# Performance work log

Hardware: AMD Instinct MI355X
Metric: run time of the kernel (lower is better)

Reference implementation:

```python
import jax, jax.numpy as jnp
import numpy as np

FEATURE_SCALE = 0.25  # cfg.feature_scale
G = 4                 # deformable/offset groups
K = 3                 # deform kernel size
KK = K * K
PAD = 1


def conv2d(x, w, b=None):
    y = jax.lax.conv_general_dilated(x, w, (1, 1), ((PAD, PAD), (PAD, PAD)),
                                     dimension_numbers=('NCHW', 'OIHW', 'NCHW'))
    return y if b is None else y + b[None, :, None, None]


def bilinear_upsample_ac(x, fs):
    # F.interpolate(mode='bilinear', align_corners=True, scale_factor=fs)
    b, c, H, W = x.shape
    Ho, Wo = H * fs, W * fs
    sy = jnp.arange(Ho, dtype=x.dtype) * ((H - 1) / (Ho - 1))
    sx = jnp.arange(Wo, dtype=x.dtype) * ((W - 1) / (Wo - 1))
    y0 = jnp.clip(jnp.floor(sy).astype(jnp.int32), 0, H - 2)
    x0 = jnp.clip(jnp.floor(sx).astype(jnp.int32), 0, W - 2)
    wy = (sy - y0)[None, None, :, None]
    wx = (sx - x0)[None, None, None, :]
    rows = x[:, :, y0, :] * (1 - wy) + x[:, :, y0 + 1, :] * wy
    return rows[:, :, :, x0] * (1 - wx) + rows[:, :, :, x0 + 1] * wx


def deform_conv(x, offset, mask, w):
    # torchvision.ops.deform_conv2d, stride 1, pad 1, weight groups = 1,
    # offset/mask groups = G. offset layout: (b, G*KK*2, H, W), (dy, dx) pairs.
    b, C, H, W = x.shape
    Cg = C // G
    off = offset.reshape(b, G, KK, 2, H, W)
    ii = (jnp.arange(KK) // K).reshape(1, 1, KK, 1, 1).astype(x.dtype)
    jj = (jnp.arange(KK) % K).reshape(1, 1, KK, 1, 1).astype(x.dtype)
    ys = jnp.arange(H, dtype=x.dtype).reshape(1, 1, 1, H, 1)
    xs = jnp.arange(W, dtype=x.dtype).reshape(1, 1, 1, 1, W)
    py = ys - PAD + ii + off[:, :, :, 0]   # (b,G,KK,H,W)
    px = xs - PAD + jj + off[:, :, :, 1]
    xt = x.reshape(b, G, Cg, H, W).transpose(0, 1, 3, 4, 2)  # (b,G,H,W,Cg)
    y0f = jnp.floor(py)
    x0f = jnp.floor(px)
    wy = py - y0f
    wx = px - x0f
    y0 = y0f.astype(jnp.int32)
    x0 = x0f.astype(jnp.int32)
    bi = jnp.arange(b).reshape(b, 1, 1, 1, 1)
    gi = jnp.arange(G).reshape(1, G, 1, 1, 1)

    def corner(yi, xi, wgt):
        valid = ((yi >= 0) & (yi < H) & (xi >= 0) & (xi < W)).astype(x.dtype)
        v = xt[bi, gi, jnp.clip(yi, 0, H - 1), jnp.clip(xi, 0, W - 1)]  # (b,G,KK,H,W,Cg)
        return v * (wgt * valid)[..., None]

    s = (corner(y0, x0, (1 - wy) * (1 - wx)) + corner(y0, x0 + 1, (1 - wy) * wx)
         + corner(y0 + 1, x0, wy * (1 - wx)) + corner(y0 + 1, x0 + 1, wy * wx))
    s = s * mask.reshape(b, G, KK, H, W)[..., None]
    wr = w.reshape(w.shape[0], G, Cg, KK)
    return jnp.einsum('bgkhwc,ogck->bohw', s, wr)


def _align(sou_list, ref_list, params):
    cat_feat, offset_vs = [], []
    for i in (3, 2, 1):
        sou, ref = sou_list[i - 1], ref_list[i - 1]
        b, C, H, W = sou.shape
        Cg = C // G
        off_w, off_b, mod_w, mod_b, reg_w = params[i]
        off_in = jnp.concatenate([sou.reshape(b, G, Cg, H, W),
                                  ref.reshape(b, G, Cg, H, W)], axis=2)
        off_in = off_in.reshape(b * G, 2 * Cg, H, W)
        offset = conv2d(off_in, off_w, off_b).reshape(b, G * 2 * KK, H, W)
        rng = min(H, W) * 0.5 / 2
        offset_map = rng * 2 * jax.nn.sigmoid(offset) - rng
        modulator = 2.0 * jax.nn.sigmoid(conv2d(sou, mod_w, mod_b))
        feat = deform_conv(sou, offset_map, modulator, reg_w)
        fs = int(1 // (FEATURE_SCALE / 2 ** (i - 1)))
        oy = jnp.mean(offset_map[:, 0::2], axis=1, keepdims=True)
        ox = jnp.mean(offset_map[:, 1::2], axis=1, keepdims=True)
        ov = bilinear_upsample_ac(jnp.concatenate([oy, ox], axis=1), fs) * fs
        cat_feat.append(feat)
        offset_vs.append(ov)
    return tuple(cat_feat) + tuple(offset_vs)


def setup_inputs() -> dict:
    key = jax.random.key(0)
    ks = jax.random.split(key, 32)
    d = {}
    shapes = {1: (2, 64, 128, 128), 2: (2, 64, 64, 64), 3: (2, 64, 32, 32)}
    k = 0
    for i in (1, 2, 3):
        d[f'sou{i}'] = jax.random.normal(ks[k], shapes[i], jnp.float32); k += 1
        d[f'ref{i}'] = jax.random.normal(ks[k], shapes[i], jnp.float32); k += 1
    Cg = 64 // G
    for i in (1, 2, 3):
        d[f'off_w{i}'] = jax.random.normal(ks[k], (2 * KK, 2 * Cg, K, K), jnp.float32) * 0.05; k += 1
        d[f'off_b{i}'] = jax.random.normal(ks[k], (2 * KK,), jnp.float32) * 0.05; k += 1
        d[f'mod_w{i}'] = jax.random.normal(ks[k], (G * KK, 64, K, K), jnp.float32) * 0.05; k += 1
        d[f'mod_b{i}'] = jax.random.normal(ks[k], (G * KK,), jnp.float32) * 0.05; k += 1
        d[f'reg_w{i}'] = jax.random.normal(ks[k], (64, 64, K, K), jnp.float32) * 0.05; k += 1
    return d


def reference(sou1, sou2, sou3, ref1, ref2, ref3,
              off_w1, off_b1, mod_w1, mod_b1, reg_w1,
              off_w2, off_b2, mod_w2, mod_b2, reg_w2,
              off_w3, off_b3, mod_w3, mod_b3, reg_w3):
    params = {1: (off_w1, off_b1, mod_w1, mod_b1, reg_w1),
              2: (off_w2, off_b2, mod_w2, mod_b2, reg_w2),
              3: (off_w3, off_b3, mod_w3, mod_b3, reg_w3)}
    return _align([sou1, sou2, sou3], [ref1, ref2, ref3], params)
```

## Files before the change

### kernel.cpp

```cpp
#include <hip/hip_runtime.h>

typedef __attribute__((ext_vector_type(8))) short short8;
typedef __attribute__((ext_vector_type(4))) float f32x4;

__device__ __forceinline__ float sigmoidf_(float x) { return 1.f / (1.f + __expf(-x)); }
__device__ __forceinline__ unsigned bf16rne(float x) {
    unsigned b = __float_as_uint(x);
    return (b + 0x7FFFu + ((b >> 16) & 1u)) >> 16;
}


struct P {
    const float *sou0, *sou1, *sou2;
    const float *ref0, *ref1, *ref2;
    const float *ob0, *ob1, *ob2;
    const float *mb0, *mb1, *mb2;
    float* out;
    float* ws;
};

union U {
    uint4 u4; int4 i4; short8 s8; f32x4 f4;
};

__global__ __launch_bounds__(256) void repack_all(
    const float* __restrict__ ow0, const float* __restrict__ mw0, const float* __restrict__ rw0,
    const float* __restrict__ ow1, const float* __restrict__ mw1, const float* __restrict__ rw1,
    const float* __restrict__ ow2, const float* __restrict__ mw2, const float* __restrict__ rw2,
    float* __restrict__ dst) {
    const int lvl = blockIdx.y;
    const float* ow = lvl == 0 ? ow0 : (lvl == 1 ? ow1 : ow2);
    const float* mw = lvl == 0 ? mw0 : (lvl == 1 ? mw1 : mw2);
    const float* rw = lvl == 0 ? rw0 : (lvl == 1 ? rw1 : rw2);
    unsigned* d = (unsigned*)(dst + lvl * 62784);
    int i = blockIdx.x * 256 + threadIdx.x;
    if (i < 18432) {
        int jw = i & 3;
        int lane = (i >> 2) & 63;
        int t3 = i >> 8;
        int ks = t3 % 18, wvu = t3 / 18;
        int o = wvu * 16 + (lane & 15);
        int c0 = ks * 32 + (lane >> 4) * 8 + 2 * jw;
        int g0 = c0 / 144, r0 = c0 % 144;
        int c1 = c0 + 1;
        int g1 = c1 / 144, r1 = c1 % 144;
        float w0 = rw[o * 576 + (g0 * 16 + (r0 & 15)) * 9 + (r0 >> 4)];
        float w1 = rw[o * 576 + (g1 * 16 + (r1 & 15)) * 9 + (r1 >> 4)];
        d[i] = bf16rne(w0) | (bf16rne(w1) << 16);
    } else if (i < 23552) {
        int o2 = i - 18432;
        int jw = o2 & 3;
        int lane = (o2 >> 2) & 63;
        int t2 = o2 >> 8;
        int nt = t2 & 1;
        int hk = t2 >> 1;
        int ks = hk % 5, h = hk / 5;
        int n = nt * 16 + (lane & 15);
        int K = ks * 32 + (lane >> 4) * 8 + 2 * jw;
        int tap = K >> 4, ch = K & 15;
        bool ok = (n < 18) && (tap < 9);
        float w0 = ok ? ow[n * 288 + (h * 16 + ch) * 9 + tap] : 0.f;
        float w1 = ok ? ow[n * 288 + (h * 16 + ch + 1) * 9 + tap] : 0.f;
        d[36864 + o2] = bf16rne(w0) | (bf16rne(w1) << 16);
    } else if (i < 37376) {
        int o3 = i - 23552;
        int jw = o3 & 3;
        int lane = (o3 >> 2) & 63;
        int t3 = o3 >> 8;
        int nt = t3 % 3, tc = t3 / 3;
        int tap = tc >> 1, c = tc & 1;
        int n = nt * 16 + (lane & 15);
        int ic0 = c * 32 + (lane >> 4) * 8 + 2 * jw;
        float w0 = (n < 36) ? mw[n * 576 + ic0 * 9 + tap] : 0.f;
        float w1 = (n < 36) ? mw[n * 576 + (ic0 + 1) * 9 + tap] : 0.f;
        d[41984 + o3] = bf16rne(w0) | (bf16rne(w1) << 16);
    }
}

__global__ __launch_bounds__(256) void k1_prep(P p) {
    __shared__ __align__(16) char smem[28512];
    const int t = blockIdx.x;
    float* ws = p.ws;
    const int tid = threadIdx.x;

    int lvl, j;
    if (t < 512) { lvl = 0; j = t; }
    else if (t < 640) { lvl = 1; j = t - 512; }
    else { lvl = 2; j = t - 640; }
    const int logW = 7 - lvl;
    const int W = 1 << logW, H = W, HW = H * W;
    const int nper = 256 >> (2 * lvl);
    const int qb = j % nper, b = j / nper;
    const int q0 = qb * 64;
    const int hlo = q0 >> logW;
    const int xlo = q0 & (W - 1);
    const int cols = (W >= 64) ? 66 : 34;
    const int rcTot = (W >= 64) ? 198 : 136;
    const float* sou = lvl == 0 ? p.sou0 : (lvl == 1 ? p.sou1 : p.sou2);
    const float* ref = lvl == 0 ? p.ref0 : (lvl == 1 ? p.ref1 : p.ref2);
    const float* base_s = sou + (size_t)b * 64 * HW;
    const float* base_r = ref + (size_t)b * 64 * HW;
    unsigned* ldsW = (unsigned*)smem;
    const bool sact = tid < rcTot;
    const int srow = tid / cols, scol = tid - srow * cols;
    const int grow = hlo - 1 + srow, gcol = xlo - 1 + scol;
    const bool inb = sact && grow >= 0 && grow < H && gcol >= 0 && gcol < W;
    const size_t goff = inb ? ((size_t)grow * W + gcol) : 0;

    float v[32];
#pragma unroll
    for (int hb = 0; hb < 2; ++hb) {
#pragma unroll
        for (int c8 = 0; c8 < 4; ++c8) {
            const float* p0 = base_s + (size_t)((hb * 4 + c8) * 8) * HW;
#pragma unroll
            for (int jj = 0; jj < 8; ++jj)
                v[c8 * 8 + jj] = inb ? p0[(size_t)jj * HW + goff] : 0.f;
        }
        if (sact) {
#pragma unroll
            for (int c8 = 0; c8 < 4; ++c8) {
                uint4 wv;
                wv.x = bf16rne(v[c8 * 8 + 0]) | (bf16rne(v[c8 * 8 + 1]) << 16);
                wv.y = bf16rne(v[c8 * 8 + 2]) | (bf16rne(v[c8 * 8 + 3]) << 16);
                wv.z = bf16rne(v[c8 * 8 + 4]) | (bf16rne(v[c8 * 8 + 5]) << 16);
                wv.w = bf16rne(v[c8 * 8 + 6]) | (bf16rne(v[c8 * 8 + 7]) << 16);
                *(uint4*)&ldsW[tid * 36 + (hb * 4 + c8) * 4] = wv;
            }
        }
    }
    __syncthreads();

    unsigned* XTb = (unsigned*)(ws + 4919232) +
                    (lvl == 0 ? 0 : (lvl == 1 ? 1048576 : 1310720));
#pragma unroll
    for (int u = 0; u < 2; ++u) {
        const int idx = tid * 2 + u;
        const int px = idx >> 3, gh = idx & 7;
        const int g = gh >> 1, half = gh & 1;
        const int rc = ((px >> logW) + 1) * cols + (px & (W - 1)) + 1;
        uint4 vv = *(const uint4*)&ldsW[rc * 36 + g * 8 + half * 4];
        *(uint4*)(XTb + ((size_t)(b * 4 + g) * HW + q0 + px) * 8 + half * 4) = vv;
    }

    const int wvu = __builtin_amdgcn_readfirstlane(tid >> 6);
    const int lane = tid & 63, quad = lane >> 4, lo16 = lane & 15;
    const int qg = q0 + wvu * 16 + lo16;
    const int rowB = (qg >> logW) - hlo;
    const int colB = (qg & (W - 1)) - xlo;
    const unsigned short* ldsS = (const unsigned short*)smem;
    const unsigned* WREPu = (const unsigned*)(ws + 4730880 + lvl * 62784);
    const unsigned* WBO2 = WREPu + 36864;
    const unsigned* WBM = WREPu + 41984;

    f32x4 accM[3], accO[4][2];
#pragma unroll
    for (int nt = 0; nt < 3; ++nt) accM[nt] = (f32x4){0.f, 0.f, 0.f, 0.f};
#pragma unroll
    for (int g = 0; g < 4; ++g)
#pragma unroll
        for (int nt = 0; nt < 2; ++nt) accO[g][nt] = (f32x4){0.f, 0.f, 0.f, 0.f};

#pragma unroll
    for (int tap = 0; tap < 9; ++tap) {
        const int ky = tap / 3, kx = tap - ky * 3;
        const int rc = (rowB + ky) * cols + colB + kx;
#pragma unroll
        for (int c = 0; c < 2; ++c) {
            U au; au.s8 = *(const short8*)&ldsS[rc * 72 + c * 32 + quad * 8];
#pragma unroll
            for (int nt = 0; nt < 3; ++nt) {
                U bu;
                bu.u4 = *(const uint4*)(WBM + (((tap * 2 + c) * 3 + nt) * 64 + lane) * 4);
                accM[nt] = __builtin_amdgcn_mfma_f32_16x16x32_bf16(au.s8, bu.s8, accM[nt], 0, 0, 0);
            }
        }
    }
#pragma unroll
    for (int ks = 0; ks < 5; ++ks) {
        const int Kbase = ks * 32 + quad * 8;
        const int tap = min(Kbase >> 4, 8);
        const int ky = tap / 3, kx = tap - ky * 3;
        const int rc = (rowB + ky) * cols + colB + kx;
        const int choff = Kbase & 15;
        U bu0, bu1;
        bu0.u4 = *(const uint4*)(WBO2 + ((ks * 2 + 0) * 64 + lane) * 4);
        bu1.u4 = *(const uint4*)(WBO2 + ((ks * 2 + 1) * 64 + lane) * 4);
#pragma unroll
        for (int g = 0; g < 4; ++g) {
            U au; au.s8 = *(const short8*)&ldsS[rc * 72 + g * 16 + choff];
            accO[g][0] = __builtin_amdgcn_mfma_f32_16x16x32_bf16(au.s8, bu0.s8, accO[g][0], 0, 0, 0);
            accO[g][1] = __builtin_amdgcn_mfma_f32_16x16x32_bf16(au.s8, bu1.s8, accO[g][1], 0, 0, 0);
        }
    }
    __syncthreads();

#pragma unroll
    for (int hb = 0; hb < 2; ++hb) {
#pragma unroll
        for (int c8 = 0; c8 < 4; ++c8) {
            const float* p0 = base_r + (size_t)((hb * 4 + c8) * 8) * HW;
#pragma unroll
            for (int jj = 0; jj < 8; ++jj)
                v[c8 * 8 + jj] = inb ? p0[(size_t)jj * HW + goff] : 0.f;
        }
        if (sact) {
#pragma unroll
            for (int c8 = 0; c8 < 4; ++c8) {
                uint4 wv;
                wv.x = bf16rne(v[c8 * 8 + 0]) | (bf16rne(v[c8 * 8 + 1]) << 16);
                wv.y = bf16rne(v[c8 * 8 + 2]) | (bf16rne(v[c8 * 8 + 3]) << 16);
                wv.z = bf16rne(v[c8 * 8 + 4]) | (bf16rne(v[c8 * 8 + 5]) << 16);
                wv.w = bf16rne(v[c8 * 8 + 6]) | (bf16rne(v[c8 * 8 + 7]) << 16);
                *(uint4*)&ldsW[tid * 36 + (hb * 4 + c8) * 4] = wv;
            }
        }
        if (hb == 0) __syncthreads();
    }
    __syncthreads();

#pragma unroll
    for (int ks = 0; ks < 5; ++ks) {
        const int Kbase = ks * 32 + quad * 8;
        const int tap = min(Kbase >> 4, 8);
        const int ky = tap / 3, kx = tap - ky * 3;
        const int rc = (rowB + ky) * cols + colB + kx;
        const int choff = Kbase & 15;
        U bu0, bu1;
        bu0.u4 = *(const uint4*)(WBO2 + (((5 + ks) * 2 + 0) * 64 + lane) * 4);
        bu1.u4 = *(const uint4*)(WBO2 + (((5 + ks) * 2 + 1) * 64 + lane) * 4);
#pragma unroll
        for (int g = 0; g < 4; ++g) {
            U au; au.s8 = *(const short8*)&ldsS[rc * 72 + g * 16 + choff];
            accO[g][0] = __builtin_amdgcn_mfma_f32_16x16x32_bf16(au.s8, bu0.s8, accO[g][0], 0, 0, 0);
            accO[g][1] = __builtin_amdgcn_mfma_f32_16x16x32_bf16(au.s8, bu1.s8, accO[g][1], 0, 0, 0);
        }
    }

    {
        const float* bias = lvl == 0 ? p.mb0 : (lvl == 1 ? p.mb1 : p.mb2);
        float* MOD = ws + (lvl == 0 ? 3096576 : (lvl == 1 ? 4276224 : 4571136));
#pragma unroll
        for (int nt = 0; nt < 3; ++nt) {
            const int o = nt * 16 + lo16;
            if (o < 36) {
                const float bb = bias[o];
                float* op = MOD + (size_t)(b * 36 + o) * HW + q0 + wvu * 16 + quad * 4;
                *(float4*)op = make_float4(2.f * sigmoidf_(accM[nt][0] + bb),
                                           2.f * sigmoidf_(accM[nt][1] + bb),
                                           2.f * sigmoidf_(accM[nt][2] + bb),
                                           2.f * sigmoidf_(accM[nt][3] + bb));
            }
        }
    }
    {
        const float* bias = lvl == 0 ? p.ob0 : (lvl == 1 ? p.ob1 : p.ob2);
        float* OFFM = ws + (lvl == 0 ? 0 : (lvl == 1 ? 2359296 : 2949120));
        const float rng = 0.25f * (float)H;
        float macc[4] = {0.f, 0.f, 0.f, 0.f};
#pragma unroll
        for (int g = 0; g < 4; ++g)
#pragma unroll
            for (int nt = 0; nt < 2; ++nt) {
                const int o = nt * 16 + lo16;
                if (o < 18) {
                    const float bb = bias[o];
                    float ovv[4];
#pragma unroll
                    for (int rg = 0; rg < 4; ++rg)
                        ovv[rg] = rng * (2.f * sigmoidf_(accO[g][nt][rg] + bb) - 1.f);
                    float* op = OFFM + (size_t)(b * 72 + g * 18 + o) * HW + q0 + wvu * 16 + quad * 4;
                    *(float4*)op = make_float4(ovv[0], ovv[1], ovv[2], ovv[3]);
#pragma unroll
                    for (int rg = 0; rg < 4; ++rg) macc[rg] += ovv[rg];
                }
            }
        const bool odd = (lo16 & 1) != 0;
        float my[4], mx[4];
#pragma unroll
        for (int rg = 0; rg < 4; ++rg) {
            my[rg] = odd ? 0.f : macc[rg];
            mx[rg] = odd ? macc[rg] : 0.f;
        }
#pragma unroll
        for (int m = 1; m < 16; m <<= 1) {
#pragma unroll
            for (int rg = 0; rg < 4; ++rg) {
                my[rg] += __shfl_xor(my[rg], m);
                mx[rg] += __shfl_xor(mx[rg], m);
            }
        }
        if (lo16 == 0) {
            float* MEAN = ws + (lvl == 0 ? 4644864 : (lvl == 1 ? 4710400 : 4726784));
            const int pxb = q0 + wvu * 16 + quad * 4;
            const float inv = 1.f / 36.f;
            *(float4*)(MEAN + (size_t)(b * 2) * HW + pxb) =
                make_float4(my[0] * inv, my[1] * inv, my[2] * inv, my[3] * inv);
            *(float4*)(MEAN + (size_t)(b * 2 + 1) * HW + pxb) =
                make_float4(mx[0] * inv, mx[1] * inv, mx[2] * inv, mx[3] * inv);
        }
    }
}

__global__ __launch_bounds__(256) void k2_fused(P p) {
    __shared__ __align__(16) unsigned lds[32 * 100];
    const int t = blockIdx.x;
    float* ws = p.ws;
    const int tid = threadIdx.x;
    if (t < 1344) {
        const int x = t & 7, r = t >> 3;
        int lvl, u;
        if (r < 128) { lvl = 0; u = x + ((r >> 1) << 3); }
        else if (r < 160) { lvl = 1; u = x + (((r - 128) >> 1) << 3); }
        else { lvl = 2; u = x + (((r - 160) >> 1) << 3); }
        const int j = 2 * u + (r & 1);
        const int logW = 7 - lvl;
        const int W = 1 << logW, H = W, HW = H * W;
        const int nper = 512 >> (2 * lvl);
        const int qb = j % nper, b = j / nper;
        const int q0 = qb * 32;
        const float* OFFM = ws + (lvl == 0 ? 0 : (lvl == 1 ? 2359296 : 2949120));
        const float* MOD = ws + (lvl == 0 ? 3096576 : (lvl == 1 ? 4276224 : 4571136));
        const unsigned* XTb = (const unsigned*)(ws + 4919232) +
                              (lvl == 0 ? 0 : (lvl == 1 ? 1048576 : 1310720));
        const unsigned* WB = (const unsigned*)(ws + 4730880 + lvl * 62784);
        float* outp = p.out + (lvl == 0 ? 655360 : (lvl == 1 ? 131072 : 0));
        const int wvu = __builtin_amdgcn_readfirstlane(tid >> 6);
        const int lane = tid & 63, quad = lane >> 4, lo16 = lane & 15;
        f32x4 acc[2];
        acc[0] = (f32x4){0.f, 0.f, 0.f, 0.f};
        acc[1] = (f32x4){0.f, 0.f, 0.f, 0.f};
        for (int c = 0; c < 3; ++c) {
            if (c) __syncthreads();
#pragma unroll
            for (int it = 0; it < 2; ++it) {
                const int task = it * 256 + tid;
                if (task < 384) {
                    const int gkl = task >> 5, px = task & 31;
                    const int gk = c * 12 + gkl;
                    const int g = gk / 9, k = gk - g * 9;
                    const int q = q0 + px;
                    const int h = q >> logW, xp = q & (W - 1);
                    const int ky = k / 3, kx = k - ky * 3;
                    float dy = OFFM[(size_t)(b * 72 + g * 18 + 2 * k) * HW + q];
                    float dx = OFFM[(size_t)(b * 72 + g * 18 + 2 * k + 1) * HW + q];
                    float m = MOD[(size_t)(b * 36 + g * 9 + k) * HW + q];
                    float py = (float)(h - 1 + ky) + dy;
                    float pxx = (float)(xp - 1 + kx) + dx;
                    float y0f = floorf(py), x0f = floorf(pxx);
                    float wy = py - y0f, wx = pxx - x0f;
                    int y0 = (int)y0f, x0 = (int)x0f;
                    const unsigned* xg = XTb + (size_t)(b * 4 + g) * HW * 8;
                    float s[16];
#pragma unroll
                    for (int cc = 0; cc < 16; ++cc) s[cc] = 0.f;
#pragma unroll
                    for (int cor = 0; cor < 4; ++cor) {
                        int yy = y0 + (cor >> 1), xx = x0 + (cor & 1);
                        float cw = ((cor >> 1) ? wy : 1.f - wy) * ((cor & 1) ? wx : 1.f - wx);
                        cw = (yy >= 0 && yy < H && xx >= 0 && xx < W) ? cw * m : 0.f;
                        int yc = min(max(yy, 0), H - 1), xc = min(max(xx, 0), W - 1);
                        const uint4* cp = (const uint4*)(xg + (size_t)((yc << logW) + xc) * 8);
                        unsigned cbuf[8];
                        *(uint4*)&cbuf[0] = cp[0];
                        *(uint4*)&cbuf[4] = cp[1];
#pragma unroll
                        for (int pr = 0; pr < 8; ++pr) {
                            float lo = __uint_as_float(cbuf[pr] << 16);
                            float hi = __uint_as_float(cbuf[pr] & 0xFFFF0000u);
                            s[2 * pr] = fmaf(cw, lo, s[2 * pr]);
                            s[2 * pr + 1] = fmaf(cw, hi, s[2 * pr + 1]);
                        }
                    }
                    unsigned* dp = &lds[px * 100 + gkl * 8];
                    uint4 w0, w1;
                    w0.x = bf16rne(s[0]) | (bf16rne(s[1]) << 16);
                    w0.y = bf16rne(s[2]) | (bf16rne(s[3]) << 16);
                    w0.z = bf16rne(s[4]) | (bf16rne(s[5]) << 16);
                    w0.w = bf16rne(s[6]) | (bf16rne(s[7]) << 16);
                    w1.x = bf16rne(s[8]) | (bf16rne(s[9]) << 16);
                    w1.y = bf16rne(s[10]) | (bf16rne(s[11]) << 16);
                    w1.z = bf16rne(s[12]) | (bf16rne(s[13]) << 16);
                    w1.w = bf16rne(s[14]) | (bf16rne(s[15]) << 16);
                    *(uint4*)dp = w0;
                    *(uint4*)(dp + 4) = w1;
                }
            }
            __syncthreads();
            uint4 bfr[6];
#pragma unroll
            for (int k6 = 0; k6 < 6; ++k6)
                bfr[k6] = *(const uint4*)(WB + (((wvu * 18 + c * 6 + k6) * 64 + lane) << 2));
#pragma unroll
            for (int k6 = 0; k6 < 6; ++k6) {
                U bu; bu.u4 = bfr[k6];
#pragma unroll
                for (int mt = 0; mt < 2; ++mt) {
                    const int px = mt * 16 + lo16;
                    U au;
                    au.u4 = *(const uint4*)&lds[px * 100 + k6 * 16 + quad * 4];
                    acc[mt] = __builtin_amdgcn_mfma_f32_16x16x32_bf16(au.s8, bu.s8, acc[mt], 0, 0, 0);
                }
            }
        }
        float* op = outp + (size_t)(b * 64 + wvu * 16 + lo16) * HW + q0;
#pragma unroll
        for (int mt = 0; mt < 2; ++mt)
#pragma unroll
            for (int rg = 0; rg < 4; ++rg)
                op[mt * 16 + quad * 4 + rg] = acc[mt][rg];
    } else {
        int flat = ((t - 1344) * 256 + tid) * 4;
        int lvl = flat >> 20;
        int r = flat & 1048575;
        int b = r >> 19, c = (r >> 18) & 1;
        int pix = r & 262143;
        int yo = pix >> 9, xo = pix & 511;
        const int H = 128 >> lvl, W = H;
        const float* MEAN = ws + (lvl == 0 ? 4644864 : (lvl == 1 ? 4710400 : 4726784));
        const float* m = MEAN + (size_t)(b * 2 + c) * H * W;
        float* o = p.out + (lvl == 0 ? 4849664 : (lvl == 1 ? 3801088 : 2752512)) +
                   ((size_t)(b * 2 + c) * 512 + yo) * 512 + xo;
        const float fs = (float)(4 << lvl);
        const float sc = (float)(H - 1) * (1.f / 511.f);
        float sy = yo * sc;
        int y0 = min((int)sy, H - 2);
        float wy = sy - (float)y0;
        float rr[4];
#pragma unroll
        for (int u = 0; u < 4; ++u) {
            float sx = (float)(xo + u) * sc;
            int x0 = min((int)sx, W - 2);
            float wx = sx - (float)x0;
            float v00 = m[y0 * W + x0], v01 = m[y0 * W + x0 + 1];
            float v10 = m[(y0 + 1) * W + x0], v11 = m[(y0 + 1) * W + x0 + 1];
            float r0 = v00 * (1.f - wy) + v10 * wy;
            float r1 = v01 * (1.f - wy) + v11 * wy;
            rr[u] = (r0 * (1.f - wx) + r1 * wx) * fs;
        }
        *(float4*)o = make_float4(rr[0], rr[1], rr[2], rr[3]);
    }
}

extern "C" void kernel_launch(void* const* d_in, const int* in_sizes, int n_in,
                              void* d_out, int out_size, void* d_ws, size_t ws_size,
                              hipStream_t stream) {
    const float* fin[21];
    for (int i = 0; i < 21; ++i) fin[i] = (const float*)d_in[i];
    P p;
    if (in_sizes[1] == in_sizes[0]) {
        p.sou0 = fin[0]; p.ref0 = fin[1];
        p.sou1 = fin[2]; p.ref1 = fin[3];
        p.sou2 = fin[4]; p.ref2 = fin[5];
    } else {
        p.sou0 = fin[0]; p.sou1 = fin[1]; p.sou2 = fin[2];
        p.ref0 = fin[3]; p.ref1 = fin[4]; p.ref2 = fin[5];
    }
    p.ob0 = fin[7]; p.mb0 = fin[9];
    p.ob1 = fin[12]; p.mb1 = fin[14];
    p.ob2 = fin[17]; p.mb2 = fin[19];
    p.out = (float*)d_out;
    p.ws = (float*)d_ws;

    repack_all<<<dim3(146, 3), 256, 0, stream>>>(
        fin[6], fin[8], fin[10], fin[11], fin[13], fin[15], fin[16], fin[18], fin[20],
        p.ws + 4730880);
    k1_prep<<<dim3(672), 256, 0, stream>>>(p);
    k2_fused<<<dim3(4416), 256, 0, stream>>>(p);
}
```

Measured before the change: 176.7 us.

## Gather all deformable samples into LDS once, then run single MFMA pass

Replaces the three-chunk gather/sync/MFMA loop in k2_fused with one phase that gathers all 36 group-tap samples per pixel into a larger LDS tile. The offset and mask loads are hoisted ahead of the bilinear gathers, and the MFMA loop then runs over all 18 k-steps. The block-to-tile mapping becomes a linear index per level, the per-element stores become vector float4 stores, and a redundant barrier in the first kernel is removed. The aim is fewer barriers and more memory-level parallelism, at the cost of more LDS per block (about 37KB), which may lower occupancy.

```diff
diff --git a/kernel.cpp b/kernel.cpp
--- a/kernel.cpp
+++ b/kernel.cpp
@@ -215,7 +215,6 @@
                 *(uint4*)&ldsW[tid * 36 + (hb * 4 + c8) * 4] = wv;
             }
         }
-        if (hb == 0) __syncthreads();
     }
     __syncthreads();
 
@@ -303,17 +302,15 @@
 }
 
 __global__ __launch_bounds__(256) void k2_fused(P p) {
-    __shared__ __align__(16) unsigned lds[32 * 100];
+    __shared__ __align__(16) unsigned lds[32 * 292];
     const int t = blockIdx.x;
     float* ws = p.ws;
     const int tid = threadIdx.x;
     if (t < 1344) {
-        const int x = t & 7, r = t >> 3;
-        int lvl, u;
-        if (r < 128) { lvl = 0; u = x + ((r >> 1) << 3); }
-        else if (r < 160) { lvl = 1; u = x + (((r - 128) >> 1) << 3); }
-        else { lvl = 2; u = x + (((r - 160) >> 1) << 3); }
-        const int j = 2 * u + (r & 1);
+        int lvl, j;
+        if (t < 1024) { lvl = 0; j = t; }
+        else if (t < 1280) { lvl = 1; j = t - 1024; }
+        else { lvl = 2; j = t - 1280; }
         const int logW = 7 - lvl;
         const int W = 1 << logW, H = W, HW = H * W;
         const int nper = 512 >> (2 * lvl);
@@ -327,88 +324,90 @@
         float* outp = p.out + (lvl == 0 ? 655360 : (lvl == 1 ? 131072 : 0));
         const int wvu = __builtin_amdgcn_readfirstlane(tid >> 6);
         const int lane = tid & 63, quad = lane >> 4, lo16 = lane & 15;
+
+        float dyv[5], dxv[5], mmv[5];
+#pragma unroll
+        for (int it = 0; it < 5; ++it) {
+            const int tsk = it * 256 + tid;
+            if (tsk < 1152) {
+                const int gk = tsk >> 5, px = tsk & 31;
+                const int g = gk / 9, k = gk - g * 9;
+                const int q = q0 + px;
+                dyv[it] = OFFM[(size_t)(b * 72 + g * 18 + 2 * k) * HW + q];
+                dxv[it] = OFFM[(size_t)(b * 72 + g * 18 + 2 * k + 1) * HW + q];
+                mmv[it] = MOD[(size_t)(b * 36 + g * 9 + k) * HW + q];
+            }
+        }
+#pragma unroll
+        for (int it = 0; it < 5; ++it) {
+            const int tsk = it * 256 + tid;
+            if (tsk < 1152) {
+                const int gk = tsk >> 5, px = tsk & 31;
+                const int g = gk / 9, k = gk - g * 9;
+                const int q = q0 + px;
+                const int h = q >> logW, xp = q & (W - 1);
+                const int ky = k / 3, kx = k - ky * 3;
+                float py = (float)(h - 1 + ky) + dyv[it];
+                float pxx = (float)(xp - 1 + kx) + dxv[it];
+                float y0f = floorf(py), x0f = floorf(pxx);
+                float wy = py - y0f, wx = pxx - x0f;
+                int y0 = (int)y0f, x0 = (int)x0f;
+                const unsigned* xg = XTb + (size_t)(b * 4 + g) * HW * 8;
+                float s[16];
+#pragma unroll
+                for (int cc = 0; cc < 16; ++cc) s[cc] = 0.f;
+#pragma unroll
+                for (int cor = 0; cor < 4; ++cor) {
+                    int yy = y0 + (cor >> 1), xx = x0 + (cor & 1);
+                    float cw = ((cor >> 1) ? wy : 1.f - wy) * ((cor & 1) ? wx : 1.f - wx);
+                    cw = (yy >= 0 && yy < H && xx >= 0 && xx < W) ? cw * mmv[it] : 0.f;
+                    int yc = min(max(yy, 0), H - 1), xc = min(max(xx, 0), W - 1);
+                    const uint4* cp = (const uint4*)(xg + (size_t)((yc << logW) + xc) * 8);
+                    unsigned cbuf[8];
+                    *(uint4*)&cbuf[0] = cp[0];
+                    *(uint4*)&cbuf[4] = cp[1];
+#pragma unroll
+                    for (int pr = 0; pr < 8; ++pr) {
+                        float lo = __uint_as_float(cbuf[pr] << 16);
+                        float hi = __uint_as_float(cbuf[pr] & 0xFFFF0000u);
+                        s[2 * pr] = fmaf(cw, lo, s[2 * pr]);
+                        s[2 * pr + 1] = fmaf(cw, hi, s[2 * pr + 1]);
+                    }
+                }
+                unsigned* dp = &lds[px * 292 + gk * 8];
+                uint4 w0, w1;
+                w0.x = bf16rne(s[0]) | (bf16rne(s[1]) << 16);
+                w0.y = bf16rne(s[2]) | (bf16rne(s[3]) << 16);
+                w0.z = bf16rne(s[4]) | (bf16rne(s[5]) << 16);
+                w0.w = bf16rne(s[6]) | (bf16rne(s[7]) << 16);
+                w1.x = bf16rne(s[8]) | (bf16rne(s[9]) << 16);
+                w1.y = bf16rne(s[10]) | (bf16rne(s[11]) << 16);
+                w1.z = bf16rne(s[12]) | (bf16rne(s[13]) << 16);
+                w1.w = bf16rne(s[14]) | (bf16rne(s[15]) << 16);
+                *(uint4*)dp = w0;
+                *(uint4*)(dp + 4) = w1;
+            }
+        }
+        __syncthreads();
+
         f32x4 acc[2];
         acc[0] = (f32x4){0.f, 0.f, 0.f, 0.f};
         acc[1] = (f32x4){0.f, 0.f, 0.f, 0.f};
-        for (int c = 0; c < 3; ++c) {
-            if (c) __syncthreads();
-#pragma unroll
-            for (int it = 0; it < 2; ++it) {
-                const int task = it * 256 + tid;
-                if (task < 384) {
-                    const int gkl = task >> 5, px = task & 31;
-                    const int gk = c * 12 + gkl;
-                    const int g = gk / 9, k = gk - g * 9;
-                    const int q = q0 + px;
-                    const int h = q >> logW, xp = q & (W - 1);
-                    const int ky = k / 3, kx = k - ky * 3;
-                    float dy = OFFM[(size_t)(b * 72 + g * 18 + 2 * k) * HW + q];
-                    float dx = OFFM[(size_t)(b * 72 + g * 18 + 2 * k + 1) * HW + q];
-                    float m = MOD[(size_t)(b * 36 + g * 9 + k) * HW + q];
-                    float py = (float)(h - 1 + ky) + dy;
-                    float pxx = (float)(xp - 1 + kx) + dx;
-                    float y0f = floorf(py), x0f = floorf(pxx);
-                    float wy = py - y0f, wx = pxx - x0f;
-                    int y0 = (int)y0f, x0 = (int)x0f;
-                    const unsigned* xg = XTb + (size_t)(b * 4 + g) * HW * 8;
-                    float s[16];
-#pragma unroll
-                    for (int cc = 0; cc < 16; ++cc) s[cc] = 0.f;
-#pragma unroll
-                    for (int cor = 0; cor < 4; ++cor) {
-                        int yy = y0 + (cor >> 1), xx = x0 + (cor & 1);
-                        float cw = ((cor >> 1) ? wy : 1.f - wy) * ((cor & 1) ? wx : 1.f - wx);
-                        cw = (yy >= 0 && yy < H && xx >= 0 && xx < W) ? cw * m : 0.f;
-                        int yc = min(max(yy, 0), H - 1), xc = min(max(xx, 0), W - 1);
-                        const uint4* cp = (const uint4*)(xg + (size_t)((yc << logW) + xc) * 8);
-                        unsigned cbuf[8];
-                        *(uint4*)&cbuf[0] = cp[0];
-                        *(uint4*)&cbuf[4] = cp[1];
-#pragma unroll
-                        for (int pr = 0; pr < 8; ++pr) {
-                            float lo = __uint_as_float(cbuf[pr] << 16);
-                            float hi = __uint_as_float(cbuf[pr] & 0xFFFF0000u);
-                            s[2 * pr] = fmaf(cw, lo, s[2 * pr]);
-                            s[2 * pr + 1] = fmaf(cw, hi, s[2 * pr + 1]);
-                        }
-                    }
-                    unsigned* dp = &lds[px * 100 + gkl * 8];
-                    uint4 w0, w1;
-                    w0.x = bf16rne(s[0]) | (bf16rne(s[1]) << 16);
-                    w0.y = bf16rne(s[2]) | (bf16rne(s[3]) << 16);
-                    w0.z = bf16rne(s[4]) | (bf16rne(s[5]) << 16);
-                    w0.w = bf16rne(s[6]) | (bf16rne(s[7]) << 16);
-                    w1.x = bf16rne(s[8]) | (bf16rne(s[9]) << 16);
-                    w1.y = bf16rne(s[10]) | (bf16rne(s[11]) << 16);
-                    w1.z = bf16rne(s[12]) | (bf16rne(s[13]) << 16);
-                    w1.w = bf16rne(s[14]) | (bf16rne(s[15]) << 16);
-                    *(uint4*)dp = w0;
-                    *(uint4*)(dp + 4) = w1;
-                }
-            }
-            __syncthreads();
-            uint4 bfr[6];
-#pragma unroll
-            for (int k6 = 0; k6 < 6; ++k6)
-                bfr[k6] = *(const uint4*)(WB + (((wvu * 18 + c * 6 + k6) * 64 + lane) << 2));
-#pragma unroll
-            for (int k6 = 0; k6 < 6; ++k6) {
-                U bu; bu.u4 = bfr[k6];
-#pragma unroll
-                for (int mt = 0; mt < 2; ++mt) {
-                    const int px = mt * 16 + lo16;
-                    U au;
-                    au.u4 = *(const uint4*)&lds[px * 100 + k6 * 16 + quad * 4];
-                    acc[mt] = __builtin_amdgcn_mfma_f32_16x16x32_bf16(au.s8, bu.s8, acc[mt], 0, 0, 0);
-                }
+#pragma unroll
+        for (int ks = 0; ks < 18; ++ks) {
+            U bu;
+            bu.u4 = *(const uint4*)(WB + (((wvu * 18 + ks) * 64 + lane) << 2));
+#pragma unroll
+            for (int mt = 0; mt < 2; ++mt) {
+                U au;
+                au.u4 = *(const uint4*)&lds[(mt * 16 + lo16) * 292 + ks * 16 + quad * 4];
+                acc[mt] = __builtin_amdgcn_mfma_f32_16x16x32_bf16(au.s8, bu.s8, acc[mt], 0, 0, 0);
             }
         }
         float* op = outp + (size_t)(b * 64 + wvu * 16 + lo16) * HW + q0;
 #pragma unroll
         for (int mt = 0; mt < 2; ++mt)
-#pragma unroll
-            for (int rg = 0; rg < 4; ++rg)
-                op[mt * 16 + quad * 4 + rg] = acc[mt][rg];
+            *(f32x4*)(op + mt * 16 + quad * 4) = acc[mt];
     } else {
         int flat = ((t - 1344) * 256 + tid) * 4;
         int lvl = flat >> 20;
```

Result: faster. 170.0 us (-3.8%).
